# Kernel tuning notes

Measured on AMD Instinct MI355X. Metric: run time of the kernel, lower is better.

The kernel has to match this reference:

```python
import jax, jax.numpy as jnp
import numpy as np

BITS_W = 2  # WAGE default weight bitwidth


def _scale(bits):
    return 2.0 ** (bits - 1)


def quantize_w(x):
    """WAGE Quantize.W: clip to [-1+delta, 1-delta], round to grid of step delta,
    with straight-through estimator for gradients."""
    s = _scale(BITS_W)
    delta = 1.0 / s
    xc = jnp.clip(x, -1.0 + delta, 1.0 - delta)
    y = jnp.round(xc * s) / s
    # straight-through: forward uses y, gradient flows as identity to x
    return x + jax.lax.stop_gradient(y - x)


def setup_inputs() -> dict:
    key = jax.random.key(0)
    k1, k2 = jax.random.split(key)
    B, D_IN, C_OUT = 16384, 1024, 1024
    inputs = jax.random.normal(k1, (B, D_IN), dtype=jnp.float32)
    # learned kernel per build(): shape [d_in, c_out]
    kernel = jax.random.normal(k2, (D_IN, C_OUT), dtype=jnp.float32) * 0.5
    return {"inputs": inputs, "kernel": kernel}


def reference(inputs, kernel):
    # quantize weights every forward pass, then dense matmul
    return jnp.matmul(inputs, quantize_w(kernel))
```

## Files before the change

kernel.cpp:

```cpp
#include <hip/hip_runtime.h>

typedef unsigned short u16;
typedef unsigned int u32;

typedef __bf16 bf16x8 __attribute__((ext_vector_type(8)));
typedef float floatx4 __attribute__((ext_vector_type(4)));


__device__ __forceinline__ u32 f2bf(float f) {
    u32 u = __builtin_bit_cast(u32, f);
    return (u + 0x7fffu + ((u >> 16) & 1u)) >> 16;
}

__device__ __forceinline__ float quant_w(float x) {
    float xc = fminf(fmaxf(x, -0.5f), 0.5f);
    return rintf(xc * 2.0f) * 0.5f;
}

__device__ __forceinline__ void gload_lds16(const u16* g, u16* l) {
    __builtin_amdgcn_global_load_lds(
        (const __attribute__((address_space(1))) void*)g,
        (__attribute__((address_space(3))) void*)l,
        16, 0, 0);
}


__global__ __launch_bounds__(256) void cast_a_kernel(const float4* __restrict__ in,
                                                     uint4* __restrict__ out) {
    int t = blockIdx.x * 256 + threadIdx.x;
    float4 a = in[2 * t];
    float4 b = in[2 * t + 1];
    uint4 o;
    o.x = f2bf(a.x) | (f2bf(a.y) << 16);
    o.y = f2bf(a.z) | (f2bf(a.w) << 16);
    o.z = f2bf(b.x) | (f2bf(b.y) << 16);
    o.w = f2bf(b.z) | (f2bf(b.w) << 16);
    out[t] = o;
}


__global__ __launch_bounds__(256) void quant_transpose_kernel(const float* __restrict__ W,
                                                              u16* __restrict__ Bt) {
    __shared__ u16 tile[32][33];
    const int KN = 1024;
    int tx = threadIdx.x;
    int ty = threadIdx.y;
    int k0 = blockIdx.y * 32;
    int n0 = blockIdx.x * 32;
#pragma unroll
    for (int i = 0; i < 4; i++) {
        int kl = ty + i * 8;
        float x = W[(k0 + kl) * KN + n0 + tx];
        tile[kl][tx] = (u16)f2bf(quant_w(x));
    }
    __syncthreads();
#pragma unroll
    for (int i = 0; i < 4; i++) {
        int nl = ty + i * 8;
        Bt[(n0 + nl) * KN + k0 + tx] = tile[tx][nl];
    }
}


__global__ __launch_bounds__(256) void gemm_bt_kernel(const u16* __restrict__ A,
                                                      const u16* __restrict__ Bt,
                                                      float* __restrict__ C) {
    const int K = 1024;
    const int N = 1024;

    __shared__ alignas(16) u16 As[128 * 64];
    __shared__ alignas(16) u16 Bs[128 * 64];

    const int tid = threadIdx.x;
    const int mbase = blockIdx.x * 128;
    const int nbase = blockIdx.y * 128;
    const int lane = tid & 63;
    const int wv = tid >> 6;
    const int wm = (wv & 1) * 64;
    const int wn = (wv >> 1) * 64;
    const int frow = lane & 15;
    const int fkc = lane >> 4;
    const int rsw = frow & 7;

    floatx4 acc[4][4] = {};

    const int srow = tid >> 3;
    const int g8 = (tid & 7) ^ (srow & 7);
    const u16* Aga[4];
    const u16* Bga[4];
#pragma unroll
    for (int q = 0; q < 4; q++) {
        Aga[q] = &A[(size_t)(mbase + q * 32 + srow) * K + g8 * 8];
        Bga[q] = &Bt[(size_t)(nbase + q * 32 + srow) * K + g8 * 8];
    }

    for (int kt = 0; kt < K; kt += 64) {
        __syncthreads();
#pragma unroll
        for (int q = 0; q < 4; q++) {
            gload_lds16(Aga[q] + kt, &As[(q * 256 + tid) * 8]);
            gload_lds16(Bga[q] + kt, &Bs[(q * 256 + tid) * 8]);
        }
        __syncthreads();

#pragma unroll
        for (int s = 0; s < 2; s++) {
            bf16x8 af[4], bf[4];
#pragma unroll
            for (int i = 0; i < 4; i++)
                af[i] = *(const bf16x8*)&As[(wm + i * 16 + frow) * 64 +
                                            (((s * 4 + fkc) ^ rsw) * 8)];
#pragma unroll
            for (int j = 0; j < 4; j++)
                bf[j] = *(const bf16x8*)&Bs[(wn + j * 16 + frow) * 64 +
                                            (((s * 4 + fkc) ^ rsw) * 8)];
#pragma unroll
            for (int i = 0; i < 4; i++)
#pragma unroll
                for (int j = 0; j < 4; j++)
                    acc[i][j] = __builtin_amdgcn_mfma_f32_16x16x32_bf16(
                        af[i], bf[j], acc[i][j], 0, 0, 0);
        }
    }

    const int crow = (lane >> 4) * 4;
    const int ccol = lane & 15;
#pragma unroll
    for (int i = 0; i < 4; i++) {
#pragma unroll
        for (int j = 0; j < 4; j++) {
            float* cp = &C[(size_t)(mbase + wm + i * 16 + crow) * N + nbase + wn + j * 16 + ccol];
#pragma unroll
            for (int r = 0; r < 4; r++) cp[r * N] = acc[i][j][r];
        }
    }
}


extern "C" void kernel_launch(void* const* d_in, const int* in_sizes, int n_in,
                              void* d_out, int out_size, void* d_ws, size_t ws_size,
                              hipStream_t stream) {
    const float* A = (const float*)d_in[0];
    const float* W = (const float*)d_in[1];
    float* C = (float*)d_out;

    u16* Abf = (u16*)d_ws;
    u16* Btq = (u16*)((char*)d_ws + (size_t)33554432);

    cast_a_kernel<<<8192, 256, 0, stream>>>((const float4*)A, (uint4*)Abf);
    quant_transpose_kernel<<<dim3(32, 32), dim3(32, 8), 0, stream>>>(W, Btq);
    gemm_bt_kernel<<<dim3(128, 8), 256, 0, stream>>>(Abf, Btq, C);
}
```

Baseline: 151.0 us.

## Double-buffer GEMM LDS with K=32 stages and software-pipelined register fragments

Rewrites the bf16 GEMM main loop to use two 128x32 LDS buffers. Global-to-LDS loads for the next K slice are issued while MFMAs run on fragments already read into registers, with ping-pong register sets, explicit vmcnt/lgkmcnt waits, one barrier per stage, and raised priority around MFMA clusters. Smaller LDS and launch bounds of (256,4) aim at higher occupancy. The cast kernel now converts two chunks per thread, halving the grid. The cost is more hand-tuned scheduling and more register pressure.

```diff
diff --git a/kernel.cpp b/kernel.cpp
--- a/kernel.cpp
+++ b/kernel.cpp
@@ -28,14 +28,17 @@
 __global__ __launch_bounds__(256) void cast_a_kernel(const float4* __restrict__ in,
                                                      uint4* __restrict__ out) {
     int t = blockIdx.x * 256 + threadIdx.x;
-    float4 a = in[2 * t];
-    float4 b = in[2 * t + 1];
-    uint4 o;
-    o.x = f2bf(a.x) | (f2bf(a.y) << 16);
-    o.y = f2bf(a.z) | (f2bf(a.w) << 16);
-    o.z = f2bf(b.x) | (f2bf(b.y) << 16);
-    o.w = f2bf(b.z) | (f2bf(b.w) << 16);
-    out[t] = o;
+#pragma unroll
+    for (int u = 0; u < 2; u++) {
+        float4 a = in[4 * t + 2 * u];
+        float4 b = in[4 * t + 2 * u + 1];
+        uint4 o;
+        o.x = f2bf(a.x) | (f2bf(a.y) << 16);
+        o.y = f2bf(a.z) | (f2bf(a.w) << 16);
+        o.z = f2bf(b.x) | (f2bf(b.y) << 16);
+        o.w = f2bf(b.z) | (f2bf(b.w) << 16);
+        out[2 * t + u] = o;
+    }
 }
 
 
@@ -62,66 +65,101 @@
 }
 
 
-__global__ __launch_bounds__(256) void gemm_bt_kernel(const u16* __restrict__ A,
-                                                      const u16* __restrict__ Bt,
-                                                      float* __restrict__ C) {
+__global__ __launch_bounds__(256, 4) void gemm_occ_kernel(const u16* __restrict__ A,
+                                                          const u16* __restrict__ Bt,
+                                                          float* __restrict__ C) {
     const int K = 1024;
     const int N = 1024;
 
-    __shared__ alignas(16) u16 As[128 * 64];
-    __shared__ alignas(16) u16 Bs[128 * 64];
+    __shared__ alignas(16) u16 As[2][128][32];
+    __shared__ alignas(16) u16 Bs[2][128][32];
 
     const int tid = threadIdx.x;
+    const int lane = tid & 63;
+    const int wid = tid >> 6;
+    const int wm = wid >> 1;
+    const int wn = wid & 1;
+    const int frow = lane & 15;
+    const int fkc = lane >> 4;
     const int mbase = blockIdx.x * 128;
     const int nbase = blockIdx.y * 128;
-    const int lane = tid & 63;
-    const int wv = tid >> 6;
-    const int wm = (wv & 1) * 64;
-    const int wn = (wv >> 1) * 64;
-    const int frow = lane & 15;
-    const int fkc = lane >> 4;
-    const int rsw = frow & 7;
+
+    const int sr = tid >> 2;
+    const int sc = tid & 3;
 
     floatx4 acc[4][4] = {};
+    bf16x8 afA[4], bfA[4], afB[4], bfB[4];
 
-    const int srow = tid >> 3;
-    const int g8 = (tid & 7) ^ (srow & 7);
-    const u16* Aga[4];
-    const u16* Bga[4];
-#pragma unroll
-    for (int q = 0; q < 4; q++) {
-        Aga[q] = &A[(size_t)(mbase + q * 32 + srow) * K + g8 * 8];
-        Bga[q] = &Bt[(size_t)(nbase + q * 32 + srow) * K + g8 * 8];
+    auto stageA = [&](int tau, int u) {
+        const int r = u * 64 + sr;
+        const int gcc = sc ^ ((r >> 1) & 3);
+        gload_lds16(&A[(size_t)(mbase + r) * K + (size_t)tau * 32 + gcc * 8],
+                    &As[tau & 1][r][sc * 8]);
+    };
+    auto stageB = [&](int tau, int u) {
+        const int r = u * 64 + sr;
+        const int gcc = sc ^ ((r >> 1) & 3);
+        gload_lds16(&Bt[(size_t)(nbase + r) * K + (size_t)tau * 32 + gcc * 8],
+                    &Bs[tau & 1][r][sc * 8]);
+    };
+
+#define LGKM0() asm volatile("s_waitcnt lgkmcnt(0)" ::: "memory")
+#define VMC(n)  asm volatile("s_waitcnt vmcnt(" #n ")" ::: "memory")
+#define BAR()                          \
+    __builtin_amdgcn_sched_barrier(0); \
+    __builtin_amdgcn_s_barrier();      \
+    __builtin_amdgcn_sched_barrier(0)
+
+#define READS(AF, BF, b)                                                             \
+    _Pragma("unroll") for (int mf = 0; mf < 4; mf++) {                               \
+        const int r = wm * 64 + mf * 16 + frow;                                      \
+        AF[mf] = *(const bf16x8*)&As[b][r][(fkc ^ ((r >> 1) & 3)) * 8];              \
+    }                                                                                \
+    _Pragma("unroll") for (int nf = 0; nf < 4; nf++) {                               \
+        const int r = wn * 64 + nf * 16 + frow;                                      \
+        BF[nf] = *(const bf16x8*)&Bs[b][r][(fkc ^ ((r >> 1) & 3)) * 8];              \
     }
 
-    for (int kt = 0; kt < K; kt += 64) {
-        __syncthreads();
-#pragma unroll
-        for (int q = 0; q < 4; q++) {
-            gload_lds16(Aga[q] + kt, &As[(q * 256 + tid) * 8]);
-            gload_lds16(Bga[q] + kt, &Bs[(q * 256 + tid) * 8]);
-        }
-        __syncthreads();
+#define MFMA_CL(AF, BF)                                                              \
+    __builtin_amdgcn_s_setprio(1);                                                   \
+    _Pragma("unroll") for (int mf = 0; mf < 4; mf++)                                 \
+        _Pragma("unroll") for (int nf = 0; nf < 4; nf++)                             \
+            acc[mf][nf] = __builtin_amdgcn_mfma_f32_16x16x32_bf16(                   \
+                AF[mf], BF[nf], acc[mf][nf], 0, 0, 0);                               \
+    __builtin_amdgcn_s_setprio(0)
 
-#pragma unroll
-        for (int s = 0; s < 2; s++) {
-            bf16x8 af[4], bf[4];
-#pragma unroll
-            for (int i = 0; i < 4; i++)
-                af[i] = *(const bf16x8*)&As[(wm + i * 16 + frow) * 64 +
-                                            (((s * 4 + fkc) ^ rsw) * 8)];
-#pragma unroll
-            for (int j = 0; j < 4; j++)
-                bf[j] = *(const bf16x8*)&Bs[(wn + j * 16 + frow) * 64 +
-                                            (((s * 4 + fkc) ^ rsw) * 8)];
-#pragma unroll
-            for (int i = 0; i < 4; i++)
-#pragma unroll
-                for (int j = 0; j < 4; j++)
-                    acc[i][j] = __builtin_amdgcn_mfma_f32_16x16x32_bf16(
-                        af[i], bf[j], acc[i][j], 0, 0, 0);
-        }
+#define REGION(tt, AFP, BFP, AFC, BFC, DOM, DOS, VN)                                 \
+    do {                                                                             \
+        if (DOS) { stageA((tt) + 1, 0); stageA((tt) + 1, 1);                         \
+                   stageB((tt) + 1, 0); stageB((tt) + 1, 1); }                       \
+        __builtin_amdgcn_sched_barrier(0);                                           \
+        if (DOM) { MFMA_CL(AFP, BFP); }                                              \
+        __builtin_amdgcn_sched_barrier(0);                                           \
+        VMC(VN);                                                                     \
+        READS(AFC, BFC, (tt) & 1)                                                    \
+        LGKM0();                                                                     \
+        BAR();                                                                       \
+    } while (0)
+
+    stageA(0, 0); stageA(0, 1); stageB(0, 0); stageB(0, 1);
+
+    REGION(0, afA, bfA, afA, bfA, false, true, 4);
+
+    for (int t = 1; t < 31; t += 2) {
+        REGION(t,     afA, bfA, afB, bfB, true, true, 4);
+        REGION(t + 1, afB, bfB, afA, bfA, true, true, 4);
     }
+
+    REGION(31, afA, bfA, afB, bfB, true, false, 0);
+
+    MFMA_CL(afB, bfB);
+
+#undef LGKM0
+#undef VMC
+#undef BAR
+#undef READS
+#undef MFMA_CL
+#undef REGION
 
     const int crow = (lane >> 4) * 4;
     const int ccol = lane & 15;
@@ -129,7 +167,8 @@
     for (int i = 0; i < 4; i++) {
 #pragma unroll
         for (int j = 0; j < 4; j++) {
-            float* cp = &C[(size_t)(mbase + wm + i * 16 + crow) * N + nbase + wn + j * 16 + ccol];
+            float* cp = &C[(size_t)(mbase + wm * 64 + i * 16 + crow) * N +
+                           nbase + wn * 64 + j * 16 + ccol];
 #pragma unroll
             for (int r = 0; r < 4; r++) cp[r * N] = acc[i][j][r];
         }
@@ -147,7 +186,7 @@
     u16* Abf = (u16*)d_ws;
     u16* Btq = (u16*)((char*)d_ws + (size_t)33554432);
 
-    cast_a_kernel<<<8192, 256, 0, stream>>>((const float4*)A, (uint4*)Abf);
+    cast_a_kernel<<<4096, 256, 0, stream>>>((const float4*)A, (uint4*)Abf);
     quant_transpose_kernel<<<dim3(32, 32), dim3(32, 8), 0, stream>>>(W, Btq);
-    gemm_bt_kernel<<<dim3(128, 8), 256, 0, stream>>>(Abf, Btq, C);
+    gemm_occ_kernel<<<dim3(128, 8), 256, 0, stream>>>(Abf, Btq, C);
 }
```

Result: slower. 159.8 us (+5.8%).
